# Kernel optimization log

Hardware: AMD Instinct MI355X
Metric: run time of the kernel (lower is better)

The kernel has to match this reference:

```python
import jax, jax.numpy as jnp
import numpy as np

HEADS = 16
D_MODEL = 1024
HEAD_DIM = D_MODEL // HEADS
NEG = -1e15


def setup_inputs() -> dict:
    key = jax.random.key(0)
    ks = jax.random.split(key, 13)
    B, L = 2, 2048
    scale = 1.0 / np.sqrt(D_MODEL)
    inp = {
        'q': jax.random.normal(ks[0], (B, L, D_MODEL), jnp.float32),
        'k': jax.random.normal(ks[1], (B, L, D_MODEL), jnp.float32),
        'v': jax.random.normal(ks[2], (B, L, D_MODEL), jnp.float32),
        'mask': jax.random.randint(ks[3], (B, 1, 1, L), 0, 2, jnp.int32),
        'Wq': jax.random.normal(ks[4], (D_MODEL, D_MODEL), jnp.float32) * scale,
        'bq': jax.random.normal(ks[5], (D_MODEL,), jnp.float32) * scale,
        'Wk': jax.random.normal(ks[6], (D_MODEL, D_MODEL), jnp.float32) * scale,
        'bk': jax.random.normal(ks[7], (D_MODEL,), jnp.float32) * scale,
        'Wv': jax.random.normal(ks[8], (D_MODEL, D_MODEL), jnp.float32) * scale,
        'bv': jax.random.normal(ks[9], (D_MODEL,), jnp.float32) * scale,
        'Wo': jax.random.normal(ks[10], (D_MODEL, D_MODEL), jnp.float32) * scale,
        'bo': jax.random.normal(ks[11], (D_MODEL,), jnp.float32) * scale,
    }
    return inp


def _split_heads(x):
    B, L, _ = x.shape
    return x.reshape(B, L, HEADS, HEAD_DIM).transpose(0, 2, 1, 3)  # [B,H,L,Dh]


def reference(q, k, v, mask, Wq, bq, Wk, bk, Wv, bv, Wo, bo):
    B, L, _ = q.shape
    # torch Linear: y = x @ W.T + b
    qh = _split_heads(q @ Wq.T + bq)
    kh = _split_heads(k @ Wk.T + bk)
    vh = _split_heads(v @ Wv.T + bv)
    scores = jnp.einsum('bhqd,bhkd->bhqk', qh, kh) / jnp.sqrt(jnp.float32(HEAD_DIM))
    scores = scores + mask.astype(scores.dtype) * NEG
    weights = jax.nn.softmax(scores, axis=-1)
    attn = jnp.einsum('bhqk,bhkd->bhqd', weights, vh)  # [B,H,L,Dh]
    attn = attn.transpose(0, 2, 1, 3).reshape(B, L, D_MODEL)
    return attn @ Wo.T + bo
```

## Files before the change

### kernel.cpp

```cpp
#include <hip/hip_runtime.h>
#include <stdint.h>

typedef __bf16 bf16;
typedef __attribute__((ext_vector_type(8))) __bf16 bf16x8;
typedef __attribute__((ext_vector_type(4))) float f32x4;

#define SEQ   2048
#define DM    1024
#define NH    16
#define HD    64
#define MROWS 4096

__device__ __forceinline__ void glds16(const bf16* g, bf16* l) {
  __builtin_amdgcn_global_load_lds(
      (__attribute__((address_space(1))) unsigned int*)(g),
      (__attribute__((address_space(3))) unsigned int*)(l),
      16, 0, 0);
}

static __device__ __forceinline__ bf16x8 cvt_f32x8(const float* __restrict__ p) {
  const f32x4 a = *(const f32x4*)p;
  const f32x4 b = *(const f32x4*)(p + 4);
  bf16x8 r;
  r[0] = (bf16)a[0]; r[1] = (bf16)a[1]; r[2] = (bf16)a[2]; r[3] = (bf16)a[3];
  r[4] = (bf16)b[0]; r[5] = (bf16)b[1]; r[6] = (bf16)b[2]; r[7] = (bf16)b[3];
  return r;
}

__global__ void conv_all(
    const float* __restrict__ q, const float* __restrict__ k, const float* __restrict__ v,
    const float* __restrict__ wq, const float* __restrict__ wk,
    const float* __restrict__ wv, const float* __restrict__ wo,
    bf16* __restrict__ dq, bf16* __restrict__ dk, bf16* __restrict__ dv,
    bf16* __restrict__ dwq, bf16* __restrict__ dwk, bf16* __restrict__ dwv,
    bf16* __restrict__ dwo)
{
  const size_t c = (size_t)blockIdx.x * 256 + threadIdx.x;
  const float* s; bf16* d; size_t off;
  if (c < 524288)        { s = q;  d = dq;  off = c; }
  else if (c < 1048576)  { s = k;  d = dk;  off = c - 524288; }
  else if (c < 1572864)  { s = v;  d = dv;  off = c - 1048576; }
  else if (c < 1703936)  { s = wq; d = dwq; off = c - 1572864; }
  else if (c < 1835008)  { s = wk; d = dwk; off = c - 1703936; }
  else if (c < 1966080)  { s = wv; d = dwv; off = c - 1835008; }
  else                   { s = wo; d = dwo; off = c - 1966080; }
  *(bf16x8*)(d + off * 8) = cvt_f32x8(s + off * 8);
}

__global__ __launch_bounds__(256, 4) void proj_qkv(
    const bf16* __restrict__ qb, const bf16* __restrict__ kb, const bf16* __restrict__ vb,
    const bf16* __restrict__ Wqb, const bf16* __restrict__ Wkb, const bf16* __restrict__ Wvb,
    const float* __restrict__ bq, const float* __restrict__ bk, const float* __restrict__ bv,
    bf16* __restrict__ Qh, bf16* __restrict__ Kh, bf16* __restrict__ Vt)
{
  __shared__ __align__(16) bf16 sA[128 * 64];
  __shared__ __align__(16) bf16 sB[128 * 64];

  const int z = blockIdx.z;
  const int o = (int)blockIdx.x + 8 * (int)blockIdx.y;
  const int rt = (o & 7) * 4 + ((o >> 3) & 3);
  const int ot = o >> 5;

  const bf16 *A, *B;
  const float* Bv;
  int m0, n0;
  if (z == 0)      { A = qb;  B = Wqb; Bv = bq; m0 = rt * 128; n0 = ot * 128; }
  else if (z == 1) { A = kb;  B = Wkb; Bv = bk; m0 = rt * 128; n0 = ot * 128; }
  else             { A = Wvb; B = vb;  Bv = bv; m0 = ot * 128; n0 = rt * 128; }

  const int tid  = threadIdx.x;
  const int lane = tid & 63;
  const int wv   = tid >> 6;
  const int quad = lane >> 4;
  const int colx = lane & 15;
  const int rm = (wv >> 1) * 64;
  const int rn = (wv & 1) * 64;

  f32x4 acc[4][4];
#pragma unroll
  for (int mi = 0; mi < 4; ++mi)
#pragma unroll
    for (int ni = 0; ni < 4; ++ni) {
      f32x4 zz = {0.f, 0.f, 0.f, 0.f};
      acc[mi][ni] = zz;
    }

  for (int kt = 0; kt < 16; ++kt) {
    const int k0 = kt * 64;
    __syncthreads();
#pragma unroll
    for (int i = 0; i < 4; ++i) {
      const int f = i * 256 + tid;
      const int row = f >> 3;
      const int cc = (f & 7) ^ (row & 7);
      glds16(A + (size_t)(m0 + row) * DM + k0 + cc * 8, sA + f * 8);
      glds16(B + (size_t)(n0 + row) * DM + k0 + cc * 8, sB + f * 8);
    }
    __syncthreads();

    bf16x8 af[4][2], bfr[4][2];
#pragma unroll
    for (int t4 = 0; t4 < 4; ++t4) {
#pragma unroll
      for (int ks = 0; ks < 2; ++ks) {
        const int ra = rm + t4 * 16 + colx;
        af[t4][ks] = *(const bf16x8*)(sA + ra * 64 + (((ks * 4 + quad) ^ (ra & 7)) * 8));
        const int rb = rn + t4 * 16 + colx;
        bfr[t4][ks] = *(const bf16x8*)(sB + rb * 64 + (((ks * 4 + quad) ^ (rb & 7)) * 8));
      }
    }
#pragma unroll
    for (int mi = 0; mi < 4; ++mi)
#pragma unroll
      for (int ni = 0; ni < 4; ++ni) {
        acc[mi][ni] = __builtin_amdgcn_mfma_f32_16x16x32_bf16(af[mi][0], bfr[ni][0], acc[mi][ni], 0, 0, 0);
        acc[mi][ni] = __builtin_amdgcn_mfma_f32_16x16x32_bf16(af[mi][1], bfr[ni][1], acc[mi][ni], 0, 0, 0);
      }
  }

  if (z == 2) {
#pragma unroll
    for (int mi = 0; mi < 4; ++mi) {
#pragma unroll
      for (int r = 0; r < 4; ++r) {
        const int m = m0 + rm + mi * 16 + quad * 4 + r;
        const float bias = Bv[m];
        const int hh = m >> 6, d = m & 63;
#pragma unroll
        for (int ni = 0; ni < 4; ++ni) {
          const int n = n0 + rn + ni * 16 + colx;
          const int b = n >> 11, l = n & 2047;
          const int lb = l >> 7, li = l & 127;
          const int perm = (li & 15) * 8 + ((li >> 4) & 7);
          Vt[(((size_t)(b * NH + hh) * HD + d) * SEQ) + lb * 128 + perm] =
              (bf16)(acc[mi][ni][r] + bias);
        }
      }
    }
  } else {
    bf16* Out = (z == 0) ? Qh : Kh;
    const float scale = (z == 0) ? 0.18033688f : 1.0f;
#pragma unroll
    for (int ni = 0; ni < 4; ++ni) {
      const int n = n0 + rn + ni * 16 + colx;
      const float bias = Bv[n];
#pragma unroll
      for (int mi = 0; mi < 4; ++mi) {
#pragma unroll
        for (int r = 0; r < 4; ++r) {
          const int m = m0 + rm + mi * 16 + quad * 4 + r;
          const float v = (acc[mi][ni][r] + bias) * scale;
          const int b = m >> 11, l = m & 2047, hh = n >> 6, d = n & 63;
          Out[((size_t)(b * NH + hh) * SEQ + l) * HD + d] = (bf16)v;
        }
      }
    }
  }
}

__global__ __launch_bounds__(256, 4) void proj_out(
    const bf16* __restrict__ At, const bf16* __restrict__ Wob,
    const float* __restrict__ bo, float* __restrict__ Out)
{
  __shared__ __align__(16) bf16 sA[128 * 64];
  __shared__ __align__(16) bf16 sB[128 * 64];

  const int o = (int)blockIdx.x + 8 * (int)blockIdx.y;
  const int m0 = ((o & 7) * 4 + ((o >> 3) & 3)) * 128;
  const int n0 = (o >> 5) * 128;

  const int tid  = threadIdx.x;
  const int lane = tid & 63;
  const int wv   = tid >> 6;
  const int quad = lane >> 4;
  const int colx = lane & 15;
  const int rm = (wv >> 1) * 64;
  const int rn = (wv & 1) * 64;

  f32x4 acc[4][4];
#pragma unroll
  for (int mi = 0; mi < 4; ++mi)
#pragma unroll
    for (int ni = 0; ni < 4; ++ni) {
      f32x4 zz = {0.f, 0.f, 0.f, 0.f};
      acc[mi][ni] = zz;
    }

  for (int kt = 0; kt < 16; ++kt) {
    const int k0 = kt * 64;
    __syncthreads();
#pragma unroll
    for (int i = 0; i < 4; ++i) {
      const int f = i * 256 + tid;
      const int row = f >> 3;
      const int cc = (f & 7) ^ (row & 7);
      glds16(At  + (size_t)(m0 + row) * DM + k0 + cc * 8, sA + f * 8);
      glds16(Wob + (size_t)(n0 + row) * DM + k0 + cc * 8, sB + f * 8);
    }
    __syncthreads();

    bf16x8 af[4][2], bfr[4][2];
#pragma unroll
    for (int t4 = 0; t4 < 4; ++t4) {
#pragma unroll
      for (int ks = 0; ks < 2; ++ks) {
        const int ra = rm + t4 * 16 + colx;
        af[t4][ks] = *(const bf16x8*)(sA + ra * 64 + (((ks * 4 + quad) ^ (ra & 7)) * 8));
        const int rb = rn + t4 * 16 + colx;
        bfr[t4][ks] = *(const bf16x8*)(sB + rb * 64 + (((ks * 4 + quad) ^ (rb & 7)) * 8));
      }
    }
#pragma unroll
    for (int mi = 0; mi < 4; ++mi)
#pragma unroll
      for (int ni = 0; ni < 4; ++ni) {
        acc[mi][ni] = __builtin_amdgcn_mfma_f32_16x16x32_bf16(af[mi][0], bfr[ni][0], acc[mi][ni], 0, 0, 0);
        acc[mi][ni] = __builtin_amdgcn_mfma_f32_16x16x32_bf16(af[mi][1], bfr[ni][1], acc[mi][ni], 0, 0, 0);
      }
  }

#pragma unroll
  for (int ni = 0; ni < 4; ++ni) {
    const int n = n0 + rn + ni * 16 + colx;
    const float bias = bo[n];
#pragma unroll
    for (int mi = 0; mi < 4; ++mi) {
#pragma unroll
      for (int r = 0; r < 4; ++r) {
        const int m = m0 + rm + mi * 16 + quad * 4 + r;
        Out[(size_t)m * DM + n] = acc[mi][ni][r] + bias;
      }
    }
  }
}

__global__ __launch_bounds__(256, 2) void attn_kernel(
    const bf16* __restrict__ Qh, const bf16* __restrict__ Kh, const bf16* __restrict__ Vt,
    const int* __restrict__ mask, bf16* __restrict__ At)
{
  __shared__ __align__(16) bf16 sK[2][128 * 64];
  __shared__ __align__(16) bf16 sV[2][64 * 128];
  __shared__ __align__(16) bf16 sP[4][16 * 128];

  const int tid  = threadIdx.x;
  const int lane = tid & 63;
  const int wv   = tid >> 6;
  const int quad = lane >> 4;
  const int colx = lane & 15;
  const int bh = blockIdx.x;
  const int b  = bh >> 4;
  const int h  = bh & 15;
  const int q0 = blockIdx.y * 128;
  const size_t base  = (size_t)bh * SEQ * HD;
  const size_t baseV = (size_t)bh * HD * SEQ;

  auto issue = [&](int K0, bf16* dK, bf16* dV) {
#pragma unroll
    for (int i = 0; i < 4; ++i) {
      const int f = i * 256 + tid;
      const int kr = f >> 3;
      const int ck = (f & 7) ^ (kr & 7);
      glds16(Kh + base + (size_t)(K0 + kr) * HD + ck * 8, dK + f * 8);
      const int dr = f >> 4;
      const int cv = (f & 15) ^ (dr & 15);
      glds16(Vt + baseV + (size_t)dr * SEQ + K0 + cv * 8, dV + f * 8);
    }
  };

  int mk[8], mkn[8];
  issue(0, sK[0], sV[0]);
#pragma unroll
  for (int nt = 0; nt < 8; ++nt)
    mk[nt] = mask[b * SEQ + nt * 16 + colx];

  bf16x8 qf[2][2];
#pragma unroll
  for (int half = 0; half < 2; ++half) {
    const int qrow = q0 + wv * 32 + half * 16 + colx;
    qf[half][0] = *(const bf16x8*)(Qh + base + (size_t)qrow * HD + quad * 8);
    qf[half][1] = *(const bf16x8*)(Qh + base + (size_t)qrow * HD + 32 + quad * 8);
  }

  f32x4 o[2][4];
  float osum[2][4];
#pragma unroll
  for (int half = 0; half < 2; ++half)
#pragma unroll
    for (int dt = 0; dt < 4; ++dt) {
      f32x4 zz = {0.f, 0.f, 0.f, 0.f};
      o[half][dt] = zz;
      osum[half][dt] = 0.f;
    }
  bf16* sPw = &sP[wv][0];

  __syncthreads();

  for (int kc = 0; kc < 16; ++kc) {
    const int cur = kc & 1;
    bf16* cK = &sK[cur][0];
    bf16* cV = &sV[cur][0];
    if (kc < 15) {
      issue((kc + 1) * 128, &sK[cur ^ 1][0], &sV[cur ^ 1][0]);
#pragma unroll
      for (int nt = 0; nt < 8; ++nt)
        mkn[nt] = mask[b * SEQ + (kc + 1) * 128 + nt * 16 + colx];
    }
    float mreg[8];
#pragma unroll
    for (int nt = 0; nt < 8; ++nt)
      mreg[nt] = (mk[nt] ? -1e30f : 0.0f) - 23.0830917f;

#pragma unroll
    for (int half = 0; half < 2; ++half) {
      f32x4 s8[8];
      __builtin_amdgcn_s_setprio(1);
#pragma unroll
      for (int nt = 0; nt < 8; ++nt) {
        f32x4 s = {0.f, 0.f, 0.f, 0.f};
        const int krow = nt * 16 + colx;
#pragma unroll
        for (int ks = 0; ks < 2; ++ks) {
          const bf16x8 kf = *(const bf16x8*)(cK + krow * 64 + (((ks * 4 + quad) ^ (krow & 7)) * 8));
          s = __builtin_amdgcn_mfma_f32_16x16x32_bf16(qf[half][ks], kf, s, 0, 0, 0);
        }
        s8[nt] = s;
      }
      __builtin_amdgcn_s_setprio(0);

      float rs[4];
#pragma unroll
      for (int r = 0; r < 4; ++r) {
        bf16x8 pk;
        float rsum = 0.f;
#pragma unroll
        for (int nt = 0; nt < 8; ++nt) {
          const float e = __builtin_amdgcn_exp2f(s8[nt][r] + mreg[nt]);
          pk[nt] = (bf16)e;
          rsum += e;
        }
        const int row = quad * 4 + r;
        *(bf16x8*)(sPw + row * 128 + ((colx ^ row) * 8)) = pk;
        rs[r] = rsum;
      }
#pragma unroll
      for (int r = 0; r < 4; ++r) {
        rs[r] += __shfl_xor(rs[r], 1);
        rs[r] += __shfl_xor(rs[r], 2);
        rs[r] += __shfl_xor(rs[r], 4);
        rs[r] += __shfl_xor(rs[r], 8);
        osum[half][r] += rs[r];
      }

      __builtin_amdgcn_s_setprio(1);
#pragma unroll
      for (int ks = 0; ks < 4; ++ks) {
        const int ch = ((ks * 4 + quad) ^ colx) * 8;
        const bf16x8 pf = *(const bf16x8*)(sPw + colx * 128 + ch);
#pragma unroll
        for (int dt = 0; dt < 4; ++dt) {
          const bf16x8 vf = *(const bf16x8*)(cV + (dt * 16 + colx) * 128 + ch);
          o[half][dt] = __builtin_amdgcn_mfma_f32_16x16x32_bf16(pf, vf, o[half][dt], 0, 0, 0);
        }
      }
      __builtin_amdgcn_s_setprio(0);
    }

    if (kc < 15) {
#pragma unroll
      for (int nt = 0; nt < 8; ++nt) mk[nt] = mkn[nt];
    }
    __syncthreads();
  }

#pragma unroll
  for (int half = 0; half < 2; ++half) {
#pragma unroll
    for (int r = 0; r < 4; ++r) {
      const float inv = 1.0f / osum[half][r];
      const int q = q0 + wv * 32 + half * 16 + quad * 4 + r;
#pragma unroll
      for (int dt = 0; dt < 4; ++dt) {
        At[((size_t)(b * SEQ + q)) * DM + h * HD + dt * 16 + colx] =
            (bf16)(o[half][dt][r] * inv);
      }
    }
  }
}

extern "C" void kernel_launch(void* const* d_in, const int* in_sizes, int n_in,
                              void* d_out, int out_size, void* d_ws, size_t ws_size,
                              hipStream_t stream) {
  (void)in_sizes; (void)n_in; (void)out_size; (void)ws_size;
  const float* q    = (const float*)d_in[0];
  const float* k    = (const float*)d_in[1];
  const float* v    = (const float*)d_in[2];
  const int*   mask = (const int*)d_in[3];
  const float* Wq   = (const float*)d_in[4];
  const float* bq   = (const float*)d_in[5];
  const float* Wk   = (const float*)d_in[6];
  const float* bk   = (const float*)d_in[7];
  const float* Wv   = (const float*)d_in[8];
  const float* bv   = (const float*)d_in[9];
  const float* Wo   = (const float*)d_in[10];
  const float* bo   = (const float*)d_in[11];
  float* out = (float*)d_out;

  const size_t T = (size_t)MROWS * DM;
  const size_t WT = (size_t)DM * DM;
  bf16* ws  = (bf16*)d_ws;
  bf16* qb  = ws;
  bf16* kb  = qb + T;
  bf16* vb  = kb + T;
  bf16* Wqb = vb + T;
  bf16* Wkb = Wqb + WT;
  bf16* Wvb = Wkb + WT;
  bf16* Wob = Wvb + WT;
  bf16* Qh  = Wob + WT;
  bf16* Kh  = Qh + T;
  bf16* Vt  = Kh + T;
  bf16* At  = qb;

  dim3 blk(256);
  conv_all<<<8192, blk, 0, stream>>>(q, k, v, Wq, Wk, Wv, Wo,
                                     qb, kb, vb, Wqb, Wkb, Wvb, Wob);
  proj_qkv<<<dim3(8, 32, 3), blk, 0, stream>>>(qb, kb, vb, Wqb, Wkb, Wvb,
                                               bq, bk, bv, Qh, Kh, Vt);
  attn_kernel<<<dim3(32, 16), blk, 0, stream>>>(Qh, Kh, Vt, mask, At);
  proj_out<<<dim3(8, 32), blk, 0, stream>>>(At, Wob, bo, out);
}
```

Measured before the change: 225.4 us.

## Share K/V fragments across both query halves and defer row-sum reduction

The QK^T loop now computes both 16-row query halves together, so each K fragment is read from LDS once and feeds two MFMAs. V fragments are loaded once per key chunk into registers and reused by both halves, removing duplicate LDS reads. The cross-lane shuffle reduction of the softmax row sums moves out of the key loop to the epilogue, since each lane's partial sums can be accumulated and reduced once at the end. The mask double-buffer is also simplified. In exchange, register pressure rises (two sets of score accumulators plus 16 V fragments), which could lower occupancy or cause spills.

```diff
diff --git a/kernel.cpp b/kernel.cpp
--- a/kernel.cpp
+++ b/kernel.cpp
@@ -267,7 +267,7 @@
     }
   };
 
-  int mk[8], mkn[8];
+  int mk[8];
   issue(0, sK[0], sV[0]);
 #pragma unroll
   for (int nt = 0; nt < 8; ++nt)
@@ -299,56 +299,64 @@
     const int cur = kc & 1;
     bf16* cK = &sK[cur][0];
     bf16* cV = &sV[cur][0];
+
+    float mreg[8];
+#pragma unroll
+    for (int nt = 0; nt < 8; ++nt)
+      mreg[nt] = (mk[nt] ? -1e30f : 0.0f) - 23.0830917f;
+
     if (kc < 15) {
       issue((kc + 1) * 128, &sK[cur ^ 1][0], &sV[cur ^ 1][0]);
 #pragma unroll
       for (int nt = 0; nt < 8; ++nt)
-        mkn[nt] = mask[b * SEQ + (kc + 1) * 128 + nt * 16 + colx];
-    }
-    float mreg[8];
-#pragma unroll
-    for (int nt = 0; nt < 8; ++nt)
-      mreg[nt] = (mk[nt] ? -1e30f : 0.0f) - 23.0830917f;
+        mk[nt] = mask[b * SEQ + (kc + 1) * 128 + nt * 16 + colx];
+    }
+
+    f32x4 s8[2][8];
+#pragma unroll
+    for (int half = 0; half < 2; ++half)
+#pragma unroll
+      for (int nt = 0; nt < 8; ++nt) {
+        f32x4 zz = {0.f, 0.f, 0.f, 0.f};
+        s8[half][nt] = zz;
+      }
+    __builtin_amdgcn_s_setprio(1);
+#pragma unroll
+    for (int nt = 0; nt < 8; ++nt) {
+      const int krow = nt * 16 + colx;
+#pragma unroll
+      for (int ks = 0; ks < 2; ++ks) {
+        const bf16x8 kf = *(const bf16x8*)(cK + krow * 64 + (((ks * 4 + quad) ^ (krow & 7)) * 8));
+        s8[0][nt] = __builtin_amdgcn_mfma_f32_16x16x32_bf16(qf[0][ks], kf, s8[0][nt], 0, 0, 0);
+        s8[1][nt] = __builtin_amdgcn_mfma_f32_16x16x32_bf16(qf[1][ks], kf, s8[1][nt], 0, 0, 0);
+      }
+    }
+    __builtin_amdgcn_s_setprio(0);
+
+    bf16x8 vf[4][4];
+#pragma unroll
+    for (int ks = 0; ks < 4; ++ks) {
+      const int ch = ((ks * 4 + quad) ^ colx) * 8;
+#pragma unroll
+      for (int dt = 0; dt < 4; ++dt)
+        vf[ks][dt] = *(const bf16x8*)(cV + (dt * 16 + colx) * 128 + ch);
+    }
 
 #pragma unroll
     for (int half = 0; half < 2; ++half) {
-      f32x4 s8[8];
-      __builtin_amdgcn_s_setprio(1);
-#pragma unroll
-      for (int nt = 0; nt < 8; ++nt) {
-        f32x4 s = {0.f, 0.f, 0.f, 0.f};
-        const int krow = nt * 16 + colx;
-#pragma unroll
-        for (int ks = 0; ks < 2; ++ks) {
-          const bf16x8 kf = *(const bf16x8*)(cK + krow * 64 + (((ks * 4 + quad) ^ (krow & 7)) * 8));
-          s = __builtin_amdgcn_mfma_f32_16x16x32_bf16(qf[half][ks], kf, s, 0, 0, 0);
-        }
-        s8[nt] = s;
-      }
-      __builtin_amdgcn_s_setprio(0);
-
-      float rs[4];
 #pragma unroll
       for (int r = 0; r < 4; ++r) {
         bf16x8 pk;
         float rsum = 0.f;
 #pragma unroll
         for (int nt = 0; nt < 8; ++nt) {
-          const float e = __builtin_amdgcn_exp2f(s8[nt][r] + mreg[nt]);
+          const float e = __builtin_amdgcn_exp2f(s8[half][nt][r] + mreg[nt]);
           pk[nt] = (bf16)e;
           rsum += e;
         }
         const int row = quad * 4 + r;
         *(bf16x8*)(sPw + row * 128 + ((colx ^ row) * 8)) = pk;
-        rs[r] = rsum;
-      }
-#pragma unroll
-      for (int r = 0; r < 4; ++r) {
-        rs[r] += __shfl_xor(rs[r], 1);
-        rs[r] += __shfl_xor(rs[r], 2);
-        rs[r] += __shfl_xor(rs[r], 4);
-        rs[r] += __shfl_xor(rs[r], 8);
-        osum[half][r] += rs[r];
+        osum[half][r] += rsum;
       }
 
       __builtin_amdgcn_s_setprio(1);
@@ -357,18 +365,12 @@
         const int ch = ((ks * 4 + quad) ^ colx) * 8;
         const bf16x8 pf = *(const bf16x8*)(sPw + colx * 128 + ch);
 #pragma unroll
-        for (int dt = 0; dt < 4; ++dt) {
-          const bf16x8 vf = *(const bf16x8*)(cV + (dt * 16 + colx) * 128 + ch);
-          o[half][dt] = __builtin_amdgcn_mfma_f32_16x16x32_bf16(pf, vf, o[half][dt], 0, 0, 0);
-        }
+        for (int dt = 0; dt < 4; ++dt)
+          o[half][dt] = __builtin_amdgcn_mfma_f32_16x16x32_bf16(pf, vf[ks][dt], o[half][dt], 0, 0, 0);
       }
       __builtin_amdgcn_s_setprio(0);
     }
 
-    if (kc < 15) {
-#pragma unroll
-      for (int nt = 0; nt < 8; ++nt) mk[nt] = mkn[nt];
-    }
     __syncthreads();
   }
 
@@ -376,7 +378,12 @@
   for (int half = 0; half < 2; ++half) {
 #pragma unroll
     for (int r = 0; r < 4; ++r) {
-      const float inv = 1.0f / osum[half][r];
+      float s = osum[half][r];
+      s += __shfl_xor(s, 1);
+      s += __shfl_xor(s, 2);
+      s += __shfl_xor(s, 4);
+      s += __shfl_xor(s, 8);
+      const float inv = 1.0f / s;
       const int q = q0 + wv * 32 + half * 16 + quad * 4 + r;
 #pragma unroll
       for (int dt = 0; dt < 4; ++dt) {
```

Result: no change. 224.2 us (-0.5%).
